# Optimization experiments

Hardware: AMD Instinct MI355X
Metric: run time of the kernel (lower is better)

The kernel has to match this reference:

```python
import jax, jax.numpy as jnp
import numpy as np

B, T, I, H, V = 128, 1024, 256, 512, 32000


def setup_inputs() -> dict:
    key = jax.random.key(0)
    ks = jax.random.split(key, 16)
    s = lambda fan_in: 1.0 / np.sqrt(fan_in)
    return {
        "x": jax.random.normal(ks[0], (B, 1, I), jnp.float32),
        "hp": jax.random.normal(ks[1], (1, B, H), jnp.float32),
        "cp": jax.random.normal(ks[2], (1, B, H), jnp.float32),
        "op": jax.random.normal(ks[3], (B, H), jnp.float32),
        "encoder_outputs": jax.random.normal(ks[4], (B, T, H), jnp.float32),
        # LSTM params (PyTorch gate order: i, f, g, o)
        "W_ih": jax.random.uniform(ks[5], (4 * H, I + H), jnp.float32, -s(H), s(H)),
        "W_hh": jax.random.uniform(ks[6], (4 * H, H), jnp.float32, -s(H), s(H)),
        "b_ih": jax.random.uniform(ks[7], (4 * H,), jnp.float32, -s(H), s(H)),
        "b_hh": jax.random.uniform(ks[8], (4 * H,), jnp.float32, -s(H), s(H)),
        # Bahdanau attention (all bias-free)
        "Wq": jax.random.uniform(ks[9], (H, H), jnp.float32, -s(H), s(H)),
        "Wm": jax.random.uniform(ks[10], (H, H), jnp.float32, -s(H), s(H)),
        "Wa": jax.random.uniform(ks[11], (1, H), jnp.float32, -s(H), s(H)),
        # output layers (bias-free)
        "Wo": jax.random.uniform(ks[12], (H, 2 * H), jnp.float32, -s(2 * H), s(2 * H)),
        "Wout": jax.random.uniform(ks[13], (V, H), jnp.float32, -s(H), s(H)),
    }


def reference(x, hp, cp, op, encoder_outputs, W_ih, W_hh, b_ih, b_hh, Wq, Wm, Wa, Wo, Wout):
    h = H  # hidden size
    # --- single-step LSTM (seq len 1) ---
    lstm_in = jnp.concatenate([x[:, 0, :], op], axis=-1)  # (B, I+H)
    gates = lstm_in @ W_ih.T + hp[0] @ W_hh.T + (b_ih + b_hh)  # (B, 4H)
    i_g = jax.nn.sigmoid(gates[:, 0 * h:1 * h])
    f_g = jax.nn.sigmoid(gates[:, 1 * h:2 * h])
    g_g = jnp.tanh(gates[:, 2 * h:3 * h])
    o_g = jax.nn.sigmoid(gates[:, 3 * h:4 * h])
    cn = f_g * cp[0] + i_g * g_g            # (B, H)
    hn = o_g * jnp.tanh(cn)                 # (B, H)

    # --- Bahdanau additive attention ---
    q = hn @ Wq.T                            # (B, H)
    k = jnp.einsum('bth,gh->btg', encoder_outputs, Wm)  # (B, T, H)
    scores = jnp.tanh(q[:, None, :] + k) @ Wa[0]         # (B, T)
    weights = jax.nn.softmax(scores, axis=1)             # softmax over time
    context = jnp.einsum('bt,btm->bm', weights, encoder_outputs)  # (B, H)

    # --- output head ---
    o_in = jnp.concatenate([hn, context], axis=1)  # (B, 2H)
    on = jnp.tanh(o_in @ Wo.T)                     # (B, H)
    output = jax.nn.log_softmax(on @ Wout.T, axis=1)  # (B, V)

    return (output, (hn[None], cn[None]), on, weights[:, None, :])
```

## Files before the change

### kernel.cpp

```cpp
#include <hip/hip_runtime.h>

#define B_ 128
#define T_ 1024
#define I_ 256
#define H_ 512
#define V_ 32000

typedef float  float4v __attribute__((ext_vector_type(4)));
typedef short  short8  __attribute__((ext_vector_type(8)));

__device__ __forceinline__ unsigned short f2bf(float f){
  unsigned int u = __float_as_uint(f);
  u += 0x7fffu + ((u >> 16) & 1u);
  return (unsigned short)(u >> 16);
}
__device__ __forceinline__ ushort4 f2bf4(float4 v){
  ushort4 u; u.x=f2bf(v.x); u.y=f2bf(v.y); u.z=f2bf(v.z); u.w=f2bf(v.w); return u;
}
__device__ __forceinline__ unsigned int cvt_pk_bf16(float lo, float hi){
  unsigned int r;
  asm volatile("v_cvt_pk_bf16_f32 %0, %1, %2" : "=v"(r) : "v"(lo), "v"(hi));
  return r;
}
__device__ __forceinline__ float fast_tanh(float x){
  float e = __expf(2.f*x);
  return 1.f - __fdividef(2.f, e + 1.f);
}
__device__ __forceinline__ float fast_sig(float x){
  return __fdividef(1.f, 1.f + __expf(-x));
}

__global__ void conv_bf16(const float4* __restrict__ src, ushort4* __restrict__ dst, int n4){
  int i = blockIdx.x*256 + threadIdx.x;
  if (i < n4) dst[i] = f2bf4(src[i]);
}

__device__ __forceinline__ const float* fetch_in(int mode, const float* a0, const float* a1,
                                                 const float* a2, int b, int k){
  if (mode == 0){
    if (k < 256)  return a0 + b*256 + k;
    if (k < 768)  return a1 + b*512 + (k-256);
    return a2 + b*512 + (k-768);
  }
  if (mode == 1) return a0 + b*512 + k;
  if (k < 512)   return a0 + b*512 + k;
  return a1 + b*512 + (k-512);
}
__device__ __forceinline__ const float* fetch_w(int mode, const float* w0, const float* w1,
                                                int n, int k){
  if (mode == 0){
    if (k < 768) return w0 + (size_t)n*768 + k;
    return w1 + (size_t)n*512 + (k-768);
  }
  if (mode == 1) return w0 + (size_t)n*512 + k;
  return w0 + (size_t)n*1024 + k;
}

__global__ void sgemm_acc(int mode,
    const float* __restrict__ a0, const float* __restrict__ a1, const float* __restrict__ a2,
    const float* __restrict__ w0, const float* __restrict__ w1,
    float* __restrict__ out, int N, int kchunk)
{
  __shared__ float inp_s[64*132];
  __shared__ float w_s[64*40];
  int tid = threadIdx.x;
  int nt = blockIdx.x, kid = blockIdx.y;
  int bg = tid & 31, ng = tid >> 5;
  int sb = tid >> 1, skof = (tid & 1)*32;
  int wn = tid & 31, wkg = tid >> 5;
  float acc[4][4] = {};
  int substeps = kchunk >> 6;

  for (int s = 0; s < substeps; ++s){
    int ks = kid*kchunk + s*64;
    __syncthreads();
    {
      const float* src = fetch_in(mode, a0, a1, a2, sb, ks + skof);
      #pragma unroll
      for (int j8 = 0; j8 < 8; ++j8){
        float4 v = ((const float4*)src)[j8];
        int kk = skof + j8*4;
        inp_s[(kk+0)*132 + sb] = v.x;
        inp_s[(kk+1)*132 + sb] = v.y;
        inp_s[(kk+2)*132 + sb] = v.z;
        inp_s[(kk+3)*132 + sb] = v.w;
      }
      int nglob = nt*32 + wn;
      const float* wsrc = fetch_w(mode, w0, w1, nglob, ks + wkg*8);
      float4 v0 = ((const float4*)wsrc)[0];
      float4 v1 = ((const float4*)wsrc)[1];
      int kk = wkg*8;
      w_s[(kk+0)*40 + wn] = v0.x;  w_s[(kk+1)*40 + wn] = v0.y;
      w_s[(kk+2)*40 + wn] = v0.z;  w_s[(kk+3)*40 + wn] = v0.w;
      w_s[(kk+4)*40 + wn] = v1.x;  w_s[(kk+5)*40 + wn] = v1.y;
      w_s[(kk+6)*40 + wn] = v1.z;  w_s[(kk+7)*40 + wn] = v1.w;
    }
    __syncthreads();
    #pragma unroll 4
    for (int k = 0; k < 64; ++k){
      float4v vb = *(const float4v*)&inp_s[k*132 + bg*4];
      float4v vw = *(const float4v*)&w_s[k*40 + ng*4];
      #pragma unroll
      for (int i = 0; i < 4; ++i)
        #pragma unroll
        for (int j = 0; j < 4; ++j)
          acc[i][j] = fmaf(vb[i], vw[j], acc[i][j]);
    }
  }
  #pragma unroll
  for (int i = 0; i < 4; ++i)
    #pragma unroll
    for (int j = 0; j < 4; ++j)
      atomicAdd(&out[(size_t)(bg*4+i)*N + nt*32 + ng*4 + j], acc[i][j]);
}

__global__ void lstm_act(const float* __restrict__ gates,
    const float* __restrict__ bih, const float* __restrict__ bhh,
    const float* __restrict__ cp, float* __restrict__ hn_out, float* __restrict__ cn_out)
{
  int i = blockIdx.x*256 + threadIdx.x;
  int b = i >> 9, h = i & 511;
  const float* g = gates + (size_t)b*2048;
  float g0 = g[h]      + bih[h]      + bhh[h];
  float g1 = g[512+h]  + bih[512+h]  + bhh[512+h];
  float g2 = g[1024+h] + bih[1024+h] + bhh[1024+h];
  float g3 = g[1536+h] + bih[1536+h] + bhh[1536+h];
  float ig = fast_sig(g0), fg = fast_sig(g1);
  float gg = fast_tanh(g2), og = fast_sig(g3);
  float cv = fg*cp[i] + ig*gg;
  float hv = og*fast_tanh(cv);
  cn_out[i] = cv;
  hn_out[i] = hv;
}

__global__ __launch_bounds__(256, 4) void attn_gemm(
    const float* __restrict__ enc, const unsigned short* __restrict__ wmbf,
    const float* __restrict__ q, const float* __restrict__ wa,
    float* __restrict__ sp)
{
  __shared__ unsigned short As[2][4096];
  __shared__ unsigned short Bs[2][4096];
  __shared__ float sred[2][128];

  int tid = threadIdx.x;
  int blk = blockIdx.x;
  int nc = blk & 3, tc = (blk >> 2) & 7, b = blk >> 5;
  int tbase = tc*128, n0 = nc*128;
  int w = tid >> 6, lane = tid & 63;
  int wm = w >> 1, wn = w & 1;
  int c = lane & 15, q4 = lane >> 4;

  float4v acc[4][4];
  #pragma unroll
  for (int i = 0; i < 4; ++i)
    #pragma unroll
    for (int j = 0; j < 4; ++j) acc[i][j] = (float4v)0.f;

  int sr = tid >> 1, sh = tid & 1;
  const float* asrc = enc + ((size_t)(b*1024 + tbase + sr))*512 + sh*16;
  const unsigned short* bsrc = wmbf + (size_t)(n0 + sr)*512 + sh*16;
  int srp = sr >> 1, sodd = sr & 1;
  int wo0 = srp*64 + ((sodd*4 + sh*2    ) ^ (srp & 7))*8;
  int wo1 = srp*64 + ((sodd*4 + sh*2 + 1) ^ (srp & 7))*8;

  int a_off[4], b_off[4];
  #pragma unroll
  for (int mi = 0; mi < 4; ++mi){
    int r = wm*64 + mi*16 + c;
    a_off[mi] = (r >> 1)*64 + (((r & 1)*4 + q4) ^ ((r >> 1) & 7))*8;
  }
  #pragma unroll
  for (int ni = 0; ni < 4; ++ni){
    int r = wn*64 + ni*16 + c;
    b_off[ni] = (r >> 1)*64 + (((r & 1)*4 + q4) ^ ((r >> 1) & 7))*8;
  }

  float4 a0, a1, a2, a3;
  uint4 bv0, bv1;

  a0 = ((const float4*)asrc)[0]; a1 = ((const float4*)asrc)[1];
  a2 = ((const float4*)asrc)[2]; a3 = ((const float4*)asrc)[3];
  bv0 = *(const uint4*)(bsrc);   bv1 = *(const uint4*)(bsrc + 8);
  {
    uint4 ca, cb;
    ca.x = cvt_pk_bf16(a0.x, a0.y); ca.y = cvt_pk_bf16(a0.z, a0.w);
    ca.z = cvt_pk_bf16(a1.x, a1.y); ca.w = cvt_pk_bf16(a1.z, a1.w);
    cb.x = cvt_pk_bf16(a2.x, a2.y); cb.y = cvt_pk_bf16(a2.z, a2.w);
    cb.z = cvt_pk_bf16(a3.x, a3.y); cb.w = cvt_pk_bf16(a3.z, a3.w);
    *(uint4*)&As[0][wo0] = ca; *(uint4*)&As[0][wo1] = cb;
    *(uint4*)&Bs[0][wo0] = bv0; *(uint4*)&Bs[0][wo1] = bv1;
  }
  a0 = ((const float4*)(asrc + 32))[0]; a1 = ((const float4*)(asrc + 32))[1];
  a2 = ((const float4*)(asrc + 32))[2]; a3 = ((const float4*)(asrc + 32))[3];
  bv0 = *(const uint4*)(bsrc + 32);     bv1 = *(const uint4*)(bsrc + 40);
  __syncthreads();

  for (int ks = 0; ks < 16; ++ks){
    int cur = ks & 1;
    if (ks < 15){
      uint4 ca, cb;
      ca.x = cvt_pk_bf16(a0.x, a0.y); ca.y = cvt_pk_bf16(a0.z, a0.w);
      ca.z = cvt_pk_bf16(a1.x, a1.y); ca.w = cvt_pk_bf16(a1.z, a1.w);
      cb.x = cvt_pk_bf16(a2.x, a2.y); cb.y = cvt_pk_bf16(a2.z, a2.w);
      cb.z = cvt_pk_bf16(a3.x, a3.y); cb.w = cvt_pk_bf16(a3.z, a3.w);
      *(uint4*)&As[cur^1][wo0] = ca; *(uint4*)&As[cur^1][wo1] = cb;
      *(uint4*)&Bs[cur^1][wo0] = bv0; *(uint4*)&Bs[cur^1][wo1] = bv1;
      if (ks < 14){
        int k0 = (ks + 2)*32;
        a0 = ((const float4*)(asrc + k0))[0]; a1 = ((const float4*)(asrc + k0))[1];
        a2 = ((const float4*)(asrc + k0))[2]; a3 = ((const float4*)(asrc + k0))[3];
        bv0 = *(const uint4*)(bsrc + k0);     bv1 = *(const uint4*)(bsrc + k0 + 8);
      }
    }
    short8 af[4];
    #pragma unroll
    for (int mi = 0; mi < 4; ++mi)
      af[mi] = *(const short8*)&As[cur][a_off[mi]];
    #pragma unroll
    for (int ni = 0; ni < 4; ++ni){
      short8 bf = *(const short8*)&Bs[cur][b_off[ni]];
      #pragma unroll
      for (int mi = 0; mi < 4; ++mi)
        acc[mi][ni] = __builtin_amdgcn_mfma_f32_16x16x32_bf16(af[mi], bf, acc[mi][ni], 0, 0, 0);
    }
    __syncthreads();
  }

  float qv[4], wv[4];
  #pragma unroll
  for (int ni = 0; ni < 4; ++ni){
    int n = n0 + wn*64 + ni*16 + c;
    qv[ni] = q[b*512 + n]; wv[ni] = wa[n];
  }
  #pragma unroll
  for (int mi = 0; mi < 4; ++mi){
    #pragma unroll
    for (int r = 0; r < 4; ++r){
      float v = 0.f;
      #pragma unroll
      for (int ni = 0; ni < 4; ++ni)
        v += wv[ni] * fast_tanh(qv[ni] + acc[mi][ni][r]);
      v += __shfl_xor(v, 1); v += __shfl_xor(v, 2);
      v += __shfl_xor(v, 4); v += __shfl_xor(v, 8);
      if (c == 0) sred[wn][wm*64 + mi*16 + q4*4 + r] = v;
    }
  }
  __syncthreads();
  if (tid < 128)
    sp[nc*131072 + b*1024 + tbase + tid] = sred[0][tid] + sred[1][tid];
}

__global__ __launch_bounds__(1024) void attn_softmax(const float* __restrict__ sp,
                                                     float* __restrict__ wf)
{
  __shared__ float red[16];
  int b = blockIdx.x, tid = threadIdx.x;
  int w = tid >> 6, lane = tid & 63;
  float s = sp[b*1024 + tid] + sp[131072 + b*1024 + tid]
          + sp[262144 + b*1024 + tid] + sp[393216 + b*1024 + tid];
  float m = s;
  m = fmaxf(m, __shfl_xor(m, 32)); m = fmaxf(m, __shfl_xor(m, 16));
  m = fmaxf(m, __shfl_xor(m, 8));  m = fmaxf(m, __shfl_xor(m, 4));
  m = fmaxf(m, __shfl_xor(m, 2));  m = fmaxf(m, __shfl_xor(m, 1));
  if (lane == 0) red[w] = m;
  __syncthreads();
  float M = red[0];
  #pragma unroll
  for (int i = 1; i < 16; ++i) M = fmaxf(M, red[i]);
  __syncthreads();
  float p = __expf(s - M);
  float t = p;
  t += __shfl_xor(t, 32); t += __shfl_xor(t, 16); t += __shfl_xor(t, 8);
  t += __shfl_xor(t, 4);  t += __shfl_xor(t, 2);  t += __shfl_xor(t, 1);
  if (lane == 0) red[w] = t;
  __syncthreads();
  float L = 0.f;
  #pragma unroll
  for (int i = 0; i < 16; ++i) L += red[i];
  wf[b*1024 + tid] = p * __fdividef(1.f, L);
}

__global__ __launch_bounds__(512) void attn_ctx(const float* __restrict__ wgt,
    const float* __restrict__ enc, float* __restrict__ ctx)
{
  __shared__ float wl[128];
  int blk = blockIdx.x;
  int b = blk >> 3, tc = blk & 7;
  int tid = threadIdx.x;
  if (tid < 128) wl[tid] = wgt[b*1024 + tc*128 + tid];
  __syncthreads();
  const float* ep = enc + ((size_t)(b*1024 + tc*128))*512 + tid;
  float a = 0.f;
  #pragma unroll 8
  for (int t2 = 0; t2 < 128; ++t2)
    a = fmaf(wl[t2], ep[(size_t)t2*512], a);
  atomicAdd(&ctx[b*512 + tid], a);
}

__global__ void tanh_act(const float* __restrict__ in, float* __restrict__ out){
  int i = blockIdx.x*256 + threadIdx.x;
  out[i] = fast_tanh(in[i]);
}

__global__ void head_gemm(const float* __restrict__ onv, const float* __restrict__ wout,
                          float* __restrict__ outp)
{
  __shared__ unsigned short As[128*40];
  __shared__ unsigned short Bs[128*40];
  int tid = threadIdx.x;
  int n0 = blockIdx.x * 128;
  int w = tid >> 6, lane = tid & 63;
  int wm = w >> 1, wn = w & 1;
  int c = lane & 15, q4 = lane >> 4;
  float4v acc[4][4];
  #pragma unroll
  for (int i = 0; i < 4; ++i)
    #pragma unroll
    for (int j = 0; j < 4; ++j) acc[i][j] = (float4v)0.f;

  int row = tid >> 1, kof = (tid & 1)*16;
  const float* sa = onv + (size_t)row*512 + kof;
  const float* sb = wout + (size_t)(n0 + row)*512 + kof;

  for (int ks = 0; ks < 16; ++ks){
    int k0 = ks*32;
    __syncthreads();
    #pragma unroll
    for (int j = 0; j < 4; ++j){
      float4 va = *(const float4*)(sa + k0 + j*4);
      *(ushort4*)&As[row*40 + kof + j*4] = f2bf4(va);
      float4 vb = *(const float4*)(sb + k0 + j*4);
      *(ushort4*)&Bs[row*40 + kof + j*4] = f2bf4(vb);
    }
    __syncthreads();
    short8 af[4];
    #pragma unroll
    for (int mi = 0; mi < 4; ++mi)
      af[mi] = *(const short8*)&As[(wm*64 + mi*16 + c)*40 + q4*8];
    #pragma unroll
    for (int ni = 0; ni < 4; ++ni){
      short8 bf = *(const short8*)&Bs[(wn*64 + ni*16 + c)*40 + q4*8];
      #pragma unroll
      for (int mi = 0; mi < 4; ++mi)
        acc[mi][ni] = __builtin_amdgcn_mfma_f32_16x16x32_bf16(af[mi], bf, acc[mi][ni], 0, 0, 0);
    }
  }
  #pragma unroll
  for (int mi = 0; mi < 4; ++mi)
    #pragma unroll
    for (int ni = 0; ni < 4; ++ni)
      #pragma unroll
      for (int r = 0; r < 4; ++r){
        int m = wm*64 + mi*16 + q4*4 + r;
        int n = n0 + wn*64 + ni*16 + c;
        outp[(size_t)m*32000 + n] = acc[mi][ni][r];
      }
}

__global__ void lse_rows(const float* __restrict__ outp, float* __restrict__ lse){
  __shared__ float rm[4], rs[4];
  int b = blockIdx.x, tid = threadIdx.x;
  int w = tid >> 6, lane = tid & 63;
  const float* row = outp + (size_t)b*32000;
  float m = -1e30f, s = 0.f;
  for (int v = tid; v < 32000; v += 256){
    float x = row[v];
    if (x > m){ s = s*__expf(m - x) + 1.f; m = x; }
    else s += __expf(x - m);
  }
  for (int off = 32; off; off >>= 1){
    float mo = __shfl_xor(m, off), so = __shfl_xor(s, off);
    float M2 = fmaxf(m, mo);
    s = s*__expf(m - M2) + so*__expf(mo - M2);
    m = M2;
  }
  if (lane == 0){ rm[w] = m; rs[w] = s; }
  __syncthreads();
  if (tid == 0){
    float M2 = fmaxf(fmaxf(rm[0], rm[1]), fmaxf(rm[2], rm[3]));
    float S = rs[0]*__expf(rm[0]-M2) + rs[1]*__expf(rm[1]-M2)
            + rs[2]*__expf(rm[2]-M2) + rs[3]*__expf(rm[3]-M2);
    lse[b] = M2 + __logf(S);
  }
}

__global__ void sub_lse(float4* outp4, const float* __restrict__ lse){
  int i = blockIdx.x*256 + threadIdx.x;
  int b = i / 8000;
  float l = lse[b];
  float4 v = outp4[i];
  v.x -= l; v.y -= l; v.z -= l; v.w -= l;
  outp4[i] = v;
}

extern "C" void kernel_launch(void* const* d_in, const int* in_sizes, int n_in,
                              void* d_out, int out_size, void* d_ws, size_t ws_size,
                              hipStream_t stream)
{
  (void)in_sizes; (void)n_in; (void)out_size; (void)ws_size;
  const float* x    = (const float*)d_in[0];
  const float* hp   = (const float*)d_in[1];
  const float* cp   = (const float*)d_in[2];
  const float* op   = (const float*)d_in[3];
  const float* enc  = (const float*)d_in[4];
  const float* Wih  = (const float*)d_in[5];
  const float* Whh  = (const float*)d_in[6];
  const float* bih  = (const float*)d_in[7];
  const float* bhh  = (const float*)d_in[8];
  const float* Wq   = (const float*)d_in[9];
  const float* Wm   = (const float*)d_in[10];
  const float* Wa   = (const float*)d_in[11];
  const float* Wo   = (const float*)d_in[12];
  const float* Wout = (const float*)d_in[13];
  float* out = (float*)d_out;

  float* ws = (float*)d_ws;
  float* gates   = ws + 0;
  float* qbuf    = ws + 262144;
  unsigned short* wmbf = (unsigned short*)(ws + 327680);
  float* spb     = ws + 458752;
  float* ctxb    = ws + 983040;
  float* oaccb   = ws + 1048576;
  float* lseb    = ws + 1114112;

  float* out_logits = out;
  float* out_hn = out + 4096000;
  float* out_cn = out + 4161536;
  float* out_on = out + 4227072;
  float* out_w  = out + 4292608;

  hipMemsetAsync(gates, 0, (size_t)(262144 + 65536)*sizeof(float), stream);
  hipMemsetAsync(ctxb, 0, (size_t)(65536 + 65536)*sizeof(float), stream);

  conv_bf16<<<256, 256, 0, stream>>>((const float4*)Wm, (ushort4*)wmbf, 65536);
  sgemm_acc<<<dim3(64, 4), 256, 0, stream>>>(0, x, op, hp, Wih, Whh, gates, 2048, 320);
  lstm_act<<<256, 256, 0, stream>>>(gates, bih, bhh, cp, out_hn, out_cn);
  sgemm_acc<<<dim3(16, 8), 256, 0, stream>>>(1, out_hn, nullptr, nullptr, Wq, nullptr, qbuf, 512, 64);
  attn_gemm<<<4096, 256, 0, stream>>>(enc, wmbf, qbuf, Wa, spb);
  attn_softmax<<<128, 1024, 0, stream>>>(spb, out_w);
  attn_ctx<<<1024, 512, 0, stream>>>(out_w, enc, ctxb);
  sgemm_acc<<<dim3(16, 8), 256, 0, stream>>>(2, out_hn, ctxb, nullptr, Wo, nullptr, oaccb, 512, 128);
  tanh_act<<<256, 256, 0, stream>>>(oaccb, out_on);
  head_gemm<<<250, 256, 0, stream>>>(out_on, Wout, out_logits);
  lse_rows<<<128, 256, 0, stream>>>(out_logits, lseb);
  sub_lse<<<4000, 256, 0, stream>>>((float4*)out_logits, lseb);
}
```

Before: 771.4 us.

## Double-buffer head GEMM with register prefetch and XCD-aware attention block mapping

Rewrites the output-head GEMM to use double-buffered LDS with an XOR-swizzled layout, register prefetch of the next K tiles and packed bf16 conversion, cutting to one barrier per K step. This lets global loads overlap with MFMA work and avoids LDS bank conflicts. The attention GEMM's block index is also remapped so that blocks sharing the same encoder tile land on the same XCD, improving L2 reuse. The cost is more registers and LDS per block.

```diff
diff --git a/kernel.cpp b/kernel.cpp
--- a/kernel.cpp
+++ b/kernel.cpp
@@ -144,7 +144,10 @@
 
   int tid = threadIdx.x;
   int blk = blockIdx.x;
-  int nc = blk & 3, tc = (blk >> 2) & 7, b = blk >> 5;
+  int xcd = blk & 7, slot = blk >> 3;
+  int tile = xcd + 8*(slot >> 2);
+  int nc = slot & 3;
+  int b = tile >> 3, tc = tile & 7;
   int tbase = tc*128, n0 = nc*128;
   int w = tid >> 6, lane = tid & 63;
   int wm = w >> 1, wn = w & 1;
@@ -302,48 +305,100 @@
   out[i] = fast_tanh(in[i]);
 }
 
-__global__ void head_gemm(const float* __restrict__ onv, const float* __restrict__ wout,
-                          float* __restrict__ outp)
-{
-  __shared__ unsigned short As[128*40];
-  __shared__ unsigned short Bs[128*40];
+__global__ __launch_bounds__(256) void head_gemm(const float* __restrict__ onv,
+    const float* __restrict__ wout, float* __restrict__ outp)
+{
+  __shared__ unsigned short As[2][4096];
+  __shared__ unsigned short Bs[2][4096];
   int tid = threadIdx.x;
   int n0 = blockIdx.x * 128;
   int w = tid >> 6, lane = tid & 63;
   int wm = w >> 1, wn = w & 1;
   int c = lane & 15, q4 = lane >> 4;
+
   float4v acc[4][4];
   #pragma unroll
   for (int i = 0; i < 4; ++i)
     #pragma unroll
     for (int j = 0; j < 4; ++j) acc[i][j] = (float4v)0.f;
 
-  int row = tid >> 1, kof = (tid & 1)*16;
-  const float* sa = onv + (size_t)row*512 + kof;
-  const float* sb = wout + (size_t)(n0 + row)*512 + kof;
+  int sr = tid >> 1, sh = tid & 1;
+  const float* asrc = onv + (size_t)sr*512 + sh*16;
+  const float* bsrc = wout + (size_t)(n0 + sr)*512 + sh*16;
+  int srp = sr >> 1, sodd = sr & 1;
+  int wo0 = srp*64 + ((sodd*4 + sh*2    ) ^ (srp & 7))*8;
+  int wo1 = srp*64 + ((sodd*4 + sh*2 + 1) ^ (srp & 7))*8;
+
+  int a_off[4], b_off[4];
+  #pragma unroll
+  for (int mi = 0; mi < 4; ++mi){
+    int r = wm*64 + mi*16 + c;
+    a_off[mi] = (r >> 1)*64 + (((r & 1)*4 + q4) ^ ((r >> 1) & 7))*8;
+  }
+  #pragma unroll
+  for (int ni = 0; ni < 4; ++ni){
+    int r = wn*64 + ni*16 + c;
+    b_off[ni] = (r >> 1)*64 + (((r & 1)*4 + q4) ^ ((r >> 1) & 7))*8;
+  }
+
+  float4 a0, a1, a2, a3, b0, b1, b2, b3;
+  a0 = ((const float4*)asrc)[0]; a1 = ((const float4*)asrc)[1];
+  a2 = ((const float4*)asrc)[2]; a3 = ((const float4*)asrc)[3];
+  b0 = ((const float4*)bsrc)[0]; b1 = ((const float4*)bsrc)[1];
+  b2 = ((const float4*)bsrc)[2]; b3 = ((const float4*)bsrc)[3];
+  {
+    uint4 ca, cb, cc, cd;
+    ca.x = cvt_pk_bf16(a0.x, a0.y); ca.y = cvt_pk_bf16(a0.z, a0.w);
+    ca.z = cvt_pk_bf16(a1.x, a1.y); ca.w = cvt_pk_bf16(a1.z, a1.w);
+    cb.x = cvt_pk_bf16(a2.x, a2.y); cb.y = cvt_pk_bf16(a2.z, a2.w);
+    cb.z = cvt_pk_bf16(a3.x, a3.y); cb.w = cvt_pk_bf16(a3.z, a3.w);
+    cc.x = cvt_pk_bf16(b0.x, b0.y); cc.y = cvt_pk_bf16(b0.z, b0.w);
+    cc.z = cvt_pk_bf16(b1.x, b1.y); cc.w = cvt_pk_bf16(b1.z, b1.w);
+    cd.x = cvt_pk_bf16(b2.x, b2.y); cd.y = cvt_pk_bf16(b2.z, b2.w);
+    cd.z = cvt_pk_bf16(b3.x, b3.y); cd.w = cvt_pk_bf16(b3.z, b3.w);
+    *(uint4*)&As[0][wo0] = ca; *(uint4*)&As[0][wo1] = cb;
+    *(uint4*)&Bs[0][wo0] = cc; *(uint4*)&Bs[0][wo1] = cd;
+  }
+  a0 = ((const float4*)(asrc + 32))[0]; a1 = ((const float4*)(asrc + 32))[1];
+  a2 = ((const float4*)(asrc + 32))[2]; a3 = ((const float4*)(asrc + 32))[3];
+  b0 = ((const float4*)(bsrc + 32))[0]; b1 = ((const float4*)(bsrc + 32))[1];
+  b2 = ((const float4*)(bsrc + 32))[2]; b3 = ((const float4*)(bsrc + 32))[3];
+  __syncthreads();
 
   for (int ks = 0; ks < 16; ++ks){
-    int k0 = ks*32;
-    __syncthreads();
-    #pragma unroll
-    for (int j = 0; j < 4; ++j){
-      float4 va = *(const float4*)(sa + k0 + j*4);
-      *(ushort4*)&As[row*40 + kof + j*4] = f2bf4(va);
-      float4 vb = *(const float4*)(sb + k0 + j*4);
-      *(ushort4*)&Bs[row*40 + kof + j*4] = f2bf4(vb);
-    }
-    __syncthreads();
+    int cur = ks & 1;
+    if (ks < 15){
+      uint4 ca, cb, cc, cd;
+      ca.x = cvt_pk_bf16(a0.x, a0.y); ca.y = cvt_pk_bf16(a0.z, a0.w);
+      ca.z = cvt_pk_bf16(a1.x, a1.y); ca.w = cvt_pk_bf16(a1.z, a1.w);
+      cb.x = cvt_pk_bf16(a2.x, a2.y); cb.y = cvt_pk_bf16(a2.z, a2.w);
+      cb.z = cvt_pk_bf16(a3.x, a3.y); cb.w = cvt_pk_bf16(a3.z, a3.w);
+      cc.x = cvt_pk_bf16(b0.x, b0.y); cc.y = cvt_pk_bf16(b0.z, b0.w);
+      cc.z = cvt_pk_bf16(b1.x, b1.y); cc.w = cvt_pk_bf16(b1.z, b1.w);
+      cd.x = cvt_pk_bf16(b2.x, b2.y); cd.y = cvt_pk_bf16(b2.z, b2.w);
+      cd.z = cvt_pk_bf16(b3.x, b3.y); cd.w = cvt_pk_bf16(b3.z, b3.w);
+      *(uint4*)&As[cur^1][wo0] = ca; *(uint4*)&As[cur^1][wo1] = cb;
+      *(uint4*)&Bs[cur^1][wo0] = cc; *(uint4*)&Bs[cur^1][wo1] = cd;
+      if (ks < 14){
+        int k0 = (ks + 2)*32;
+        a0 = ((const float4*)(asrc + k0))[0]; a1 = ((const float4*)(asrc + k0))[1];
+        a2 = ((const float4*)(asrc + k0))[2]; a3 = ((const float4*)(asrc + k0))[3];
+        b0 = ((const float4*)(bsrc + k0))[0]; b1 = ((const float4*)(bsrc + k0))[1];
+        b2 = ((const float4*)(bsrc + k0))[2]; b3 = ((const float4*)(bsrc + k0))[3];
+      }
+    }
     short8 af[4];
     #pragma unroll
     for (int mi = 0; mi < 4; ++mi)
-      af[mi] = *(const short8*)&As[(wm*64 + mi*16 + c)*40 + q4*8];
+      af[mi] = *(const short8*)&As[cur][a_off[mi]];
     #pragma unroll
     for (int ni = 0; ni < 4; ++ni){
-      short8 bf = *(const short8*)&Bs[(wn*64 + ni*16 + c)*40 + q4*8];
+      short8 bf = *(const short8*)&Bs[cur][b_off[ni]];
       #pragma unroll
       for (int mi = 0; mi < 4; ++mi)
         acc[mi][ni] = __builtin_amdgcn_mfma_f32_16x16x32_bf16(af[mi], bf, acc[mi][ni], 0, 0, 0);
     }
+    __syncthreads();
   }
   #pragma unroll
   for (int mi = 0; mi < 4; ++mi)
```

New measurement: 729.5 us. 1.06x faster.
